# Kernel optimization log

Hardware: AMD Instinct MI355X
Metric: run time of the kernel (lower is better)

## Reference

```python
import jax, jax.numpy as jnp
import numpy as np

B = 2048   # batch
C = 64     # EEG channels (num_eegch)
T = 125    # time samples -> pool5 -> 25 -> (p=5, 5)
H = 8      # num_heads
L = 6      # num_layers
D = 16     # num_projected_features
QK = 8     # qkv_len
P = 5      # tokens before cls
EPS = 1e-5


def setup_inputs() -> dict:
    key = jax.random.key(0)
    ks = iter(jax.random.split(key, 64))

    def nrm(shape, s=0.05):
        return jax.random.normal(next(ks), shape, jnp.float32) * s

    return {
        "x": jax.random.normal(next(ks), (B, 1, C, T), jnp.float32),
        "conv_t_w": nrm((8, 1, 1, 63)),
        "conv_t_b": nrm((8,)),
        "bn1_g": 1.0 + nrm((8,)),
        "bn1_b": nrm((8,)),
        "bn1_m": nrm((8,)),
        "bn1_v": 1.0 + 0.1 * jax.random.uniform(next(ks), (8,), jnp.float32),
        "conv_s_w": nrm((16, 1, C, 1)),
        "conv_s_b": nrm((16,)),
        "bn2_g": 1.0 + nrm((16,)),
        "bn2_b": nrm((16,)),
        "bn2_m": nrm((16,)),
        "bn2_v": 1.0 + 0.1 * jax.random.uniform(next(ks), (16,), jnp.float32),
        "proj_w": nrm((D, 16 * 5)),
        "proj_b": nrm((D,)),
        "cls_token": nrm((1, 1, D), 1.0),
        "pe": nrm((1, P + 1, D), 1.0),
        "qkv_w": nrm((L, 3 * H * QK, D)),
        "qkv_b": nrm((L, 3 * H * QK)),
        "out_w": nrm((L, D, H * QK)),
        "out_b": nrm((L, D)),
        "ln1_g": jnp.ones((L, D), jnp.float32),
        "ln1_b": jnp.zeros((L, D), jnp.float32),
        "ln2_g": jnp.ones((L, D), jnp.float32),
        "ln2_b": jnp.zeros((L, D), jnp.float32),
        "mlp_w1": nrm((L, 2 * D, D)),
        "mlp_b1": nrm((L, 2 * D)),
        "mlp_w2": nrm((L, D, 2 * D)),
        "mlp_b2": nrm((L, D)),
        "head_ln_g": jnp.ones((D,), jnp.float32),
        "head_ln_b": jnp.zeros((D,), jnp.float32),
        "head_w": nrm((2, D)),
        "head_b": nrm((2,)),
    }


def _bn(z, g, b, m, v):
    s = (g * jax.lax.rsqrt(v + EPS))[None, :, None, None]
    return (z - m[None, :, None, None]) * s + b[None, :, None, None]


def _ln(z, g, b):
    m = z.mean(-1, keepdims=True)
    var = jnp.mean((z - m) ** 2, -1, keepdims=True)
    return (z - m) * jax.lax.rsqrt(var + EPS) * g + b


def _forward(x, conv_t_w, conv_t_b, bn1_g, bn1_b, bn1_m, bn1_v,
             conv_s_w, conv_s_b, bn2_g, bn2_b, bn2_m, bn2_v,
             proj_w, proj_b, cls_token, pe,
             qkv_w, qkv_b, out_w, out_b, ln1_g, ln1_b, ln2_g, ln2_b,
             mlp_w1, mlp_b1, mlp_w2, mlp_b2,
             head_ln_g, head_ln_b, head_w, head_b):
    b = x.shape[0]
    dn = ('NCHW', 'OIHW', 'NCHW')
    # temporal conv, 'same' padding on width (kernel 63 -> pad 31/31)
    y = jax.lax.conv_general_dilated(x, conv_t_w, (1, 1), [(0, 0), (31, 31)], dimension_numbers=dn)
    y = _bn(y + conv_t_b[None, :, None, None], bn1_g, bn1_b, bn1_m, bn1_v)
    # grouped spatial conv collapses the EEG-channel axis
    y = jax.lax.conv_general_dilated(y, conv_s_w, (1, 1), 'VALID', dimension_numbers=dn, feature_group_count=8)
    y = _bn(y + conv_s_b[None, :, None, None], bn2_g, bn2_b, bn2_m, bn2_v)
    y = jax.nn.elu(y)                              # (b,16,1,125)
    y = y.reshape(b, 16, 1, T // 5, 5).mean(-1)    # avg_pool2d (1,5) -> (b,16,1,25)
    # dropout: identity at inference
    y = y.reshape(b, 16, 1, P, 5)
    y = jnp.swapaxes(y, 3, 4)
    tok = jnp.swapaxes(y.reshape(b, 16 * 5, P), 1, 2)   # (b,5,80)
    tok = tok @ proj_w.T + proj_b                       # (b,5,16)
    z = jnp.concatenate([jnp.broadcast_to(cls_token, (b, 1, D)), tok], axis=1) + pe  # (b,6,16)
    scale = QK ** -0.5
    for i in range(L):
        h1 = _ln(z, ln1_g[i], ln1_b[i])
        qkv = h1 @ qkv_w[i].T + qkv_b[i]                # (b,6,3*H*QK)
        q, k, v = jnp.split(qkv, 3, axis=-1)
        q = q.reshape(b, P + 1, H, QK).transpose(0, 2, 1, 3)
        k = k.reshape(b, P + 1, H, QK).transpose(0, 2, 1, 3)
        v = v.reshape(b, P + 1, H, QK).transpose(0, 2, 1, 3)
        att = jax.nn.softmax(jnp.einsum('bhsd,bhtd->bhst', q, k) * scale, axis=-1)
        o = jnp.einsum('bhst,bhtd->bhsd', att, v).transpose(0, 2, 1, 3).reshape(b, P + 1, H * QK)
        z = o @ out_w[i].T + out_b[i] + z
        h2 = _ln(z, ln2_g[i], ln2_b[i])
        m = jax.nn.gelu(h2 @ mlp_w1[i].T + mlp_b1[i], approximate=False) @ mlp_w2[i].T + mlp_b2[i]
        z = m + z
    cls = _ln(z[:, 0, :], head_ln_g, head_ln_b)
    return jax.nn.softmax(cls @ head_w.T + head_b, axis=-1)


def reference(x, conv_t_w, conv_t_b, bn1_g, bn1_b, bn1_m, bn1_v,
              conv_s_w, conv_s_b, bn2_g, bn2_b, bn2_m, bn2_v,
              proj_w, proj_b, cls_token, pe,
              qkv_w, qkv_b, out_w, out_b, ln1_g, ln1_b, ln2_g, ln2_b,
              mlp_w1, mlp_b1, mlp_w2, mlp_b2,
              head_ln_g, head_ln_b, head_w, head_b):
    return _forward(x, conv_t_w, conv_t_b, bn1_g, bn1_b, bn1_m, bn1_v,
                    conv_s_w, conv_s_b, bn2_g, bn2_b, bn2_m, bn2_v,
                    proj_w, proj_b, cls_token, pe,
                    qkv_w, qkv_b, out_w, out_b, ln1_g, ln1_b, ln2_g, ln2_b,
                    mlp_w1, mlp_b1, mlp_w2, mlp_b2,
                    head_ln_g, head_ln_b, head_w, head_b)
```

## Files before the change

kernel.cpp:

```cpp
#include <hip/hip_runtime.h>

#define TB 256

#define WAVE_SYNC() do { asm volatile("" ::: "memory"); \
                         __builtin_amdgcn_wave_barrier(); \
                         asm volatile("" ::: "memory"); } while (0)

#define WQKV 0
#define BQKV 3840
#define WOUT 4032
#define BOUT 5120
#define WM1  5136
#define BM1  5776
#define WM2  5808
#define BM2  6384
#define LN1G 6400
#define LN1B 6416
#define LN2G 6432
#define LN2B 6448
#define WEND 6464
#define SSTR 1568
#define SH1  0
#define SQKV 128
#define SMHS 1312
#define LDS_TOT (WEND + 2*SSTR)
#define FSTR 3664
#define FXSP  0
#define FPOOL 3136
#define FTOK  3584

__device__ __forceinline__ float ln_norm16(float z, float g, float bb) {
    float s = z, q = z * z;
    #pragma unroll
    for (int off = 8; off >= 1; off >>= 1) {
        s += __shfl_xor(s, off, 16);
        q += __shfl_xor(q, off, 16);
    }
    float mean = s * 0.0625f;
    float var  = q * 0.0625f - mean * mean;
    return (z - mean) * rsqrtf(var + 1e-5f) * g + bb;
}

__device__ __forceinline__ float gelu_exact(float a) {
    float xa = fabsf(a) * 0.70710678118654752f;
    float tt = 1.f / (1.f + 0.3275911f * xa);
    float poly = tt * (0.254829592f + tt * (-0.284496736f + tt * (1.421413741f
               + tt * (-1.453152027f + tt * 1.061405429f))));
    float erfv = 1.f - poly * __expf(-xa * xa);
    erfv = a >= 0.f ? erfv : -erfv;
    return 0.5f * a * (1.f + erfv);
}

__device__ __forceinline__ float dot16(const float* h, float4 w0, float4 w1,
                                       float4 w2, float4 w3) {
    return h[0]*w0.x + h[1]*w0.y + h[2]*w0.z + h[3]*w0.w
         + h[4]*w1.x + h[5]*w1.y + h[6]*w1.z + h[7]*w1.w
         + h[8]*w2.x + h[9]*w2.y + h[10]*w2.z + h[11]*w2.w
         + h[12]*w3.x + h[13]*w3.y + h[14]*w3.z + h[15]*w3.w;
}

extern "C" __global__ __launch_bounds__(TB, 2)
void eegnet_vit_fused(
    const float* __restrict__ x,
    const float* __restrict__ conv_t_w, const float* __restrict__ conv_t_b,
    const float* __restrict__ bn1_g, const float* __restrict__ bn1_b,
    const float* __restrict__ bn1_m, const float* __restrict__ bn1_v,
    const float* __restrict__ conv_s_w, const float* __restrict__ conv_s_b,
    const float* __restrict__ bn2_g, const float* __restrict__ bn2_b,
    const float* __restrict__ bn2_m, const float* __restrict__ bn2_v,
    const float* __restrict__ proj_w, const float* __restrict__ proj_b,
    const float* __restrict__ cls_token, const float* __restrict__ pe,
    const float* __restrict__ qkv_w, const float* __restrict__ qkv_b,
    const float* __restrict__ out_w, const float* __restrict__ out_b,
    const float* __restrict__ ln1_g, const float* __restrict__ ln1_b,
    const float* __restrict__ ln2_g, const float* __restrict__ ln2_b,
    const float* __restrict__ mlp_w1, const float* __restrict__ mlp_b1,
    const float* __restrict__ mlp_w2, const float* __restrict__ mlp_b2,
    const float* __restrict__ head_ln_g, const float* __restrict__ head_ln_b,
    const float* __restrict__ head_w, const float* __restrict__ head_b,
    float* __restrict__ out)
{
    __shared__ __align__(16) float sm[LDS_TOT];
    const int tid = threadIdx.x;
    const int ss  = tid >> 7;
    const int u   = tid & 127;
    const int b2  = blockIdx.x * 2 + ss;
    float* smf = sm + ss * FSTR;

    for (int i = u; i < 16 * 71; i += 128) {
        int row = i / 71, k = i - row * 71;
        int off = (k < 32) ? k : (k + 125);
        smf[FXSP + row * 196 + off] = 0.f;
    }

    {
        const float* xb = x + (size_t)b2 * 8000;
        const int t = min(u, 124);
        float a0[16];
        #pragma unroll
        for (int o = 0; o < 16; ++o) a0[o] = 0.f;
        #pragma unroll 8
        for (int c = 0; c < 64; ++c) {
            float xv = xb[c * 125 + t];
            #pragma unroll
            for (int o = 0; o < 16; ++o)
                a0[o] += conv_s_w[o * 64 + c] * xv;
        }
        if (u < 125) {
            #pragma unroll
            for (int o = 0; o < 16; ++o)
                smf[FXSP + o * 196 + 32 + t] = a0[o];
        }
    }

    const int oo = u & 15, qg = u >> 4, gg = oo >> 1;
    float sa, cc;
    {
        float s1 = bn1_g[gg] * rsqrtf(bn1_v[gg] + 1e-5f);
        float b1 = (conv_t_b[gg] - bn1_m[gg]) * s1 + bn1_b[gg];
        float s2 = bn2_g[oo] * rsqrtf(bn2_v[oo] + 1e-5f);
        float ssum = 0.f;
        const float4* csw = reinterpret_cast<const float4*>(conv_s_w + oo * 64);
        #pragma unroll
        for (int i = 0; i < 16; ++i) {
            float4 v = csw[i];
            ssum += v.x + v.y + v.z + v.w;
        }
        sa = s1 * s2;
        cc = (b1 * ssum + conv_s_b[oo] - bn2_m[oo]) * s2 + bn2_b[oo];
    }
    float wt[63];
    #pragma unroll
    for (int k = 0; k < 63; ++k) wt[k] = conv_t_w[gg * 63 + k];

    __syncthreads();

    #pragma unroll 1
    for (int jj = 0; jj < 4; ++jj) {
        int j = qg + 8 * jj;
        if (j < 25) {
            int base = FXSP + oo * 196 + 5 * j + 1;
            float acc5[5] = {0.f, 0.f, 0.f, 0.f, 0.f};
            #pragma unroll
            for (int m = 0; m < 67; ++m) {
                float xv = smf[base + m];
                #pragma unroll
                for (int uu = 0; uu < 5; ++uu)
                    if (uu <= m && m - uu <= 62) acc5[uu] += wt[m - uu] * xv;
            }
            float psum = 0.f;
            #pragma unroll
            for (int uu = 0; uu < 5; ++uu) {
                float v = acc5[uu] * sa + cc;
                psum += (v > 0.f) ? v : (__expf(v) - 1.f);
            }
            smf[FPOOL + oo * 28 + j] = psum * 0.2f;
        }
    }

    __syncthreads();

    if (u < 80) {
        int p = u >> 4, dd = u & 15;
        float acc = proj_b[dd];
        const float4* wp = reinterpret_cast<const float4*>(proj_w + dd * 80);
        #pragma unroll
        for (int i = 0; i < 20; ++i) {
            float4 w4 = wp[i];
            acc += w4.x * smf[FPOOL + ((4*i+0)/5) * 28 + p * 5 + ((4*i+0)%5)];
            acc += w4.y * smf[FPOOL + ((4*i+1)/5) * 28 + p * 5 + ((4*i+1)%5)];
            acc += w4.z * smf[FPOOL + ((4*i+2)/5) * 28 + p * 5 + ((4*i+2)%5)];
            acc += w4.w * smf[FPOOL + ((4*i+3)/5) * 28 + p * 5 + ((4*i+3)%5)];
        }
        smf[FTOK + p * 16 + dd] = acc;
    }

    __syncthreads();

    const int d16 = u & 15;
    const int t6c = min(qg, 5);
    float z = ((t6c == 0) ? cls_token[d16] : smf[FTOK + (t6c - 1) * 16 + d16])
            + pe[t6c * 16 + d16];

    const int sb   = WEND + ss * SSTR;
    const int wav  = u >> 6;
    const int al   = u & 63;

    #pragma unroll 1
    for (int li = 0; li < 6; ++li) {
        __syncthreads();

        {
            const float4* s1 = reinterpret_cast<const float4*>(qkv_w + li * 3072);
            #pragma unroll
            for (int it = 0; it < 3; ++it) {
                int i = tid + it * 256;
                float4 v = s1[i];
                int j = i >> 2, k = (i & 3) << 2;
                *reinterpret_cast<float4*>(&sm[WQKV + j * 20 + k]) = v;
            }
            {
                float4 v = reinterpret_cast<const float4*>(out_w + li * 1024)[tid];
                int j = tid >> 4, k = (tid & 15) << 2;
                *reinterpret_cast<float4*>(&sm[WOUT + j * 68 + k]) = v;
            }
            if (tid < 128) {
                float4 v = reinterpret_cast<const float4*>(mlp_w1 + li * 512)[tid];
                int j = tid >> 2, k = (tid & 3) << 2;
                *reinterpret_cast<float4*>(&sm[WM1 + j * 20 + k]) = v;
            } else {
                int i = tid - 128;
                float4 v = reinterpret_cast<const float4*>(mlp_w2 + li * 512)[i];
                int j = i >> 3, k = (i & 7) << 2;
                *reinterpret_cast<float4*>(&sm[WM2 + j * 36 + k]) = v;
            }
            if (tid < 192) sm[BQKV + tid] = qkv_b[li * 192 + tid];
            else if (tid < 208) sm[BOUT + tid - 192] = out_b[li * 16 + tid - 192];
            else if (tid < 240) sm[BM1 + tid - 208]  = mlp_b1[li * 32 + tid - 208];
            else               sm[BM2 + tid - 240]  = mlp_b2[li * 16 + tid - 240];
            if (tid >= 64 && tid < 80)        sm[LN1G + tid - 64]  = ln1_g[li * 16 + tid - 64];
            else if (tid >= 80 && tid < 96)   sm[LN1B + tid - 80]  = ln1_b[li * 16 + tid - 80];
            else if (tid >= 96 && tid < 112)  sm[LN2G + tid - 96]  = ln2_g[li * 16 + tid - 96];
            else if (tid >= 112 && tid < 128) sm[LN2B + tid - 112] = ln2_b[li * 16 + tid - 112];
        }
        __syncthreads();

        sm[sb + SH1 + t6c * 20 + d16] = ln_norm16(z, sm[LN1G + d16], sm[LN1B + d16]);
        WAVE_SYNC();

        float hr[16];
        {
            const float4* pA = reinterpret_cast<const float4*>(&sm[sb + SH1 + t6c * 20]);
            #pragma unroll
            for (int i = 0; i < 4; ++i) {
                float4 va = pA[i];
                hr[4*i+0] = va.x; hr[4*i+1] = va.y; hr[4*i+2] = va.z; hr[4*i+3] = va.w;
            }
        }

        #pragma unroll 2
        for (int r = 0; r < 12; ++r) {
            int j = d16 + 16 * r;
            const float4* wp = reinterpret_cast<const float4*>(&sm[WQKV + j * 20]);
            float4 w0 = wp[0], w1_ = wp[1], w2_ = wp[2], w3_ = wp[3];
            sm[sb + SQKV + t6c * 196 + j] = sm[BQKV + j] + dot16(hr, w0, w1_, w2_, w3_);
        }
        __syncthreads();

        {
            bool act = (wav == 0) ? (al < 32) : (al < 16);
            if (act) {
                int h  = al & 7;
                int qs = (wav == 0) ? (al >> 3) : 4 + (al >> 3);
                const int qoff = sb + SQKV + qs * 196 + h * 8;
                const float4* qp = reinterpret_cast<const float4*>(&sm[qoff]);
                float4 q0 = qp[0], q1 = qp[1];
                float sc[6];
                #pragma unroll
                for (int t = 0; t < 6; ++t) {
                    const float4* kp = reinterpret_cast<const float4*>(&sm[sb + SQKV + t * 196 + 64 + h * 8]);
                    float4 k0 = kp[0], k1 = kp[1];
                    sc[t] = (q0.x*k0.x + q0.y*k0.y + q0.z*k0.z + q0.w*k0.w
                           + q1.x*k1.x + q1.y*k1.y + q1.z*k1.z + q1.w*k1.w)
                           * 0.35355339059327373f;
                }
                float mx = sc[0];
                #pragma unroll
                for (int t = 1; t < 6; ++t) mx = fmaxf(mx, sc[t]);
                float ssum = 0.f;
                #pragma unroll
                for (int t = 0; t < 6; ++t) { sc[t] = __expf(sc[t] - mx); ssum += sc[t]; }
                float inv = 1.f / ssum;
                float o0=0.f,o1=0.f,o2=0.f,o3=0.f,o4=0.f,o5=0.f,o6=0.f,o7=0.f;
                #pragma unroll
                for (int t = 0; t < 6; ++t) {
                    const float4* vp = reinterpret_cast<const float4*>(&sm[sb + SQKV + t * 196 + 128 + h * 8]);
                    float4 v0 = vp[0], v1 = vp[1];
                    float a = sc[t] * inv;
                    o0 += a*v0.x; o1 += a*v0.y; o2 += a*v0.z; o3 += a*v0.w;
                    o4 += a*v1.x; o5 += a*v1.y; o6 += a*v1.z; o7 += a*v1.w;
                }
                *reinterpret_cast<float4*>(&sm[qoff    ]) = float4{o0,o1,o2,o3};
                *reinterpret_cast<float4*>(&sm[qoff + 4]) = float4{o4,o5,o6,o7};
            }
        }
        WAVE_SYNC();

        {
            const float4* wop = reinterpret_cast<const float4*>(&sm[WOUT + d16 * 68]);
            const float4* oa  = reinterpret_cast<const float4*>(&sm[sb + SQKV + t6c * 196]);
            float acc = sm[BOUT + d16];
            #pragma unroll 4
            for (int i = 0; i < 16; ++i) {
                float4 w = wop[i];
                float4 va = oa[i];
                acc += va.x*w.x + va.y*w.y + va.z*w.z + va.w*w.w;
            }
            z += acc;
        }

        sm[sb + SH1 + t6c * 20 + d16] = ln_norm16(z, sm[LN2G + d16], sm[LN2B + d16]);
        WAVE_SYNC();
        {
            const float4* pA = reinterpret_cast<const float4*>(&sm[sb + SH1 + t6c * 20]);
            #pragma unroll
            for (int i = 0; i < 4; ++i) {
                float4 va = pA[i];
                hr[4*i+0] = va.x; hr[4*i+1] = va.y; hr[4*i+2] = va.z; hr[4*i+3] = va.w;
            }
        }

        #pragma unroll
        for (int r = 0; r < 2; ++r) {
            int uu = d16 + 16 * r;
            const float4* wp = reinterpret_cast<const float4*>(&sm[WM1 + uu * 20]);
            float4 w0 = wp[0], w1_ = wp[1], w2_ = wp[2], w3_ = wp[3];
            float a = sm[BM1 + uu] + dot16(hr, w0, w1_, w2_, w3_);
            sm[sb + SMHS + t6c * 36 + uu] = gelu_exact(a);
        }
        WAVE_SYNC();

        {
            const float4* wp = reinterpret_cast<const float4*>(&sm[WM2 + d16 * 36]);
            const float4* mA = reinterpret_cast<const float4*>(&sm[sb + SMHS + t6c * 36]);
            float acc = sm[BM2 + d16];
            #pragma unroll
            for (int i = 0; i < 8; ++i) {
                float4 w = wp[i];
                float4 va = mA[i];
                acc += va.x*w.x + va.y*w.y + va.z*w.z + va.w*w.w;
            }
            z += acc;
        }
    }

    if (u < 16) {
        float cv = ln_norm16(z, head_ln_g[d16], head_ln_b[d16]);
        float p0 = cv * head_w[d16];
        float p1 = cv * head_w[16 + d16];
        #pragma unroll
        for (int off = 8; off >= 1; off >>= 1) {
            p0 += __shfl_xor(p0, off, 16);
            p1 += __shfl_xor(p1, off, 16);
        }
        if (u == 0) {
            float l0 = p0 + head_b[0], l1 = p1 + head_b[1];
            float mx = fmaxf(l0, l1);
            float e0 = __expf(l0 - mx), e1 = __expf(l1 - mx);
            float inv = 1.f / (e0 + e1);
            out[b2 * 2 + 0] = e0 * inv;
            out[b2 * 2 + 1] = e1 * inv;
        }
    }
}

extern "C" void kernel_launch(void* const* d_in, const int* in_sizes, int n_in,
                              void* d_out, int out_size, void* d_ws, size_t ws_size,
                              hipStream_t stream) {
    (void)n_in; (void)d_ws; (void)ws_size; (void)out_size;
    const float* a0  = (const float*)d_in[0];
    const float* a1  = (const float*)d_in[1];
    const float* a2  = (const float*)d_in[2];
    const float* a3  = (const float*)d_in[3];
    const float* a4  = (const float*)d_in[4];
    const float* a5  = (const float*)d_in[5];
    const float* a6  = (const float*)d_in[6];
    const float* a7  = (const float*)d_in[7];
    const float* a8  = (const float*)d_in[8];
    const float* a9  = (const float*)d_in[9];
    const float* a10 = (const float*)d_in[10];
    const float* a11 = (const float*)d_in[11];
    const float* a12 = (const float*)d_in[12];
    const float* a13 = (const float*)d_in[13];
    const float* a14 = (const float*)d_in[14];
    const float* a15 = (const float*)d_in[15];
    const float* a16 = (const float*)d_in[16];
    const float* a17 = (const float*)d_in[17];
    const float* a18 = (const float*)d_in[18];
    const float* a19 = (const float*)d_in[19];
    const float* a20 = (const float*)d_in[20];
    const float* a21 = (const float*)d_in[21];
    const float* a22 = (const float*)d_in[22];
    const float* a23 = (const float*)d_in[23];
    const float* a24 = (const float*)d_in[24];
    const float* a25 = (const float*)d_in[25];
    const float* a26 = (const float*)d_in[26];
    const float* a27 = (const float*)d_in[27];
    const float* a28 = (const float*)d_in[28];
    const float* a29 = (const float*)d_in[29];
    const float* a30 = (const float*)d_in[30];
    const float* a31 = (const float*)d_in[31];
    const float* a32 = (const float*)d_in[32];

    int Bn = in_sizes[0] / (64 * 125);
    eegnet_vit_fused<<<Bn / 2, TB, 0, stream>>>(
        a0, a1, a2, a3, a4, a5, a6, a7, a8, a9, a10, a11, a12, a13, a14, a15, a16,
        a17, a18, a19, a20, a21, a22, a23, a24, a25, a26, a27, a28, a29, a30, a31, a32,
        (float*)d_out);
}
```

Baseline: 248.4 us.

## Split frontend into separate kernel and process two samples per thread in transformer

The fused kernel becomes two launches. A frontend kernel with one sample per 128-thread block writes projected tokens to workspace. A transformer kernel then handles four samples per 256-thread block, with each thread computing two samples so every weight read from LDS is reused twice. The goal is to amortize the per-layer weight staging into LDS and the shared-memory weight reads over more samples, and to size each stage's occupancy on its own. The cost is an extra launch, a global round trip for the tokens, and higher register pressure from keeping two sample states per thread.

```diff
diff --git a/kernel.cpp b/kernel.cpp
--- a/kernel.cpp
+++ b/kernel.cpp
@@ -1,10 +1,147 @@
 #include <hip/hip_runtime.h>
-
-#define TB 256
 
 #define WAVE_SYNC() do { asm volatile("" ::: "memory"); \
                          __builtin_amdgcn_wave_barrier(); \
                          asm volatile("" ::: "memory"); } while (0)
+
+__device__ __forceinline__ float ln_norm16(float z, float g, float bb) {
+    float s = z, q = z * z;
+    #pragma unroll
+    for (int off = 8; off >= 1; off >>= 1) {
+        s += __shfl_xor(s, off, 16);
+        q += __shfl_xor(q, off, 16);
+    }
+    float mean = s * 0.0625f;
+    float var  = q * 0.0625f - mean * mean;
+    return (z - mean) * rsqrtf(var + 1e-5f) * g + bb;
+}
+
+__device__ __forceinline__ float gelu_exact(float a) {
+    float xa = fabsf(a) * 0.70710678118654752f;
+    float tt = 1.f / (1.f + 0.3275911f * xa);
+    float poly = tt * (0.254829592f + tt * (-0.284496736f + tt * (1.421413741f
+               + tt * (-1.453152027f + tt * 1.061405429f))));
+    float erfv = 1.f - poly * __expf(-xa * xa);
+    erfv = a >= 0.f ? erfv : -erfv;
+    return 0.5f * a * (1.f + erfv);
+}
+
+__device__ __forceinline__ float dot16(const float* h, float4 w0, float4 w1,
+                                       float4 w2, float4 w3) {
+    return h[0]*w0.x + h[1]*w0.y + h[2]*w0.z + h[3]*w0.w
+         + h[4]*w1.x + h[5]*w1.y + h[6]*w1.z + h[7]*w1.w
+         + h[8]*w2.x + h[9]*w2.y + h[10]*w2.z + h[11]*w2.w
+         + h[12]*w3.x + h[13]*w3.y + h[14]*w3.z + h[15]*w3.w;
+}
+
+#define FXSP  0
+#define FPOOL 3136
+#define F_TOT 3584
+
+extern "C" __global__ __launch_bounds__(128, 2)
+void eegnet_frontend(
+    const float* __restrict__ x,
+    const float* __restrict__ conv_t_w, const float* __restrict__ conv_t_b,
+    const float* __restrict__ bn1_g, const float* __restrict__ bn1_b,
+    const float* __restrict__ bn1_m, const float* __restrict__ bn1_v,
+    const float* __restrict__ conv_s_w, const float* __restrict__ conv_s_b,
+    const float* __restrict__ bn2_g, const float* __restrict__ bn2_b,
+    const float* __restrict__ bn2_m, const float* __restrict__ bn2_v,
+    const float* __restrict__ proj_w, const float* __restrict__ proj_b,
+    float* __restrict__ tokws)
+{
+    __shared__ __align__(16) float sm[F_TOT];
+    const int b   = blockIdx.x;
+    const int tid = threadIdx.x;
+
+    for (int i = tid; i < 16 * 71; i += 128) {
+        int row = i / 71, k = i - row * 71;
+        int off = (k < 32) ? k : (k + 125);
+        sm[FXSP + row * 196 + off] = 0.f;
+    }
+
+    {
+        const float* xb = x + (size_t)b * 8000;
+        const int t = min(tid, 124);
+        float a0[16];
+        #pragma unroll
+        for (int o = 0; o < 16; ++o) a0[o] = 0.f;
+        #pragma unroll 8
+        for (int c = 0; c < 64; ++c) {
+            float xv = xb[c * 125 + t];
+            #pragma unroll
+            for (int o = 0; o < 16; ++o)
+                a0[o] += conv_s_w[o * 64 + c] * xv;
+        }
+        if (tid < 125) {
+            #pragma unroll
+            for (int o = 0; o < 16; ++o)
+                sm[FXSP + o * 196 + 32 + t] = a0[o];
+        }
+    }
+
+    const int oo = tid & 15, qg = tid >> 4, gg = oo >> 1;
+    float sa, cc;
+    {
+        float s1 = bn1_g[gg] * rsqrtf(bn1_v[gg] + 1e-5f);
+        float b1 = (conv_t_b[gg] - bn1_m[gg]) * s1 + bn1_b[gg];
+        float s2 = bn2_g[oo] * rsqrtf(bn2_v[oo] + 1e-5f);
+        float ssum = 0.f;
+        const float4* csw = reinterpret_cast<const float4*>(conv_s_w + oo * 64);
+        #pragma unroll
+        for (int i = 0; i < 16; ++i) {
+            float4 v = csw[i];
+            ssum += v.x + v.y + v.z + v.w;
+        }
+        sa = s1 * s2;
+        cc = (b1 * ssum + conv_s_b[oo] - bn2_m[oo]) * s2 + bn2_b[oo];
+    }
+    float wt[63];
+    #pragma unroll
+    for (int k = 0; k < 63; ++k) wt[k] = conv_t_w[gg * 63 + k];
+
+    __syncthreads();
+
+    #pragma unroll 1
+    for (int jj = 0; jj < 4; ++jj) {
+        int j = qg + 8 * jj;
+        if (j < 25) {
+            int base = FXSP + oo * 196 + 5 * j + 1;
+            float acc5[5] = {0.f, 0.f, 0.f, 0.f, 0.f};
+            #pragma unroll
+            for (int m = 0; m < 67; ++m) {
+                float xv = sm[base + m];
+                #pragma unroll
+                for (int uu = 0; uu < 5; ++uu)
+                    if (uu <= m && m - uu <= 62) acc5[uu] += wt[m - uu] * xv;
+            }
+            float psum = 0.f;
+            #pragma unroll
+            for (int uu = 0; uu < 5; ++uu) {
+                float v = acc5[uu] * sa + cc;
+                psum += (v > 0.f) ? v : (__expf(v) - 1.f);
+            }
+            sm[FPOOL + oo * 28 + j] = psum * 0.2f;
+        }
+    }
+
+    __syncthreads();
+
+    if (tid < 80) {
+        int p = tid >> 4, dd = tid & 15;
+        float acc = proj_b[dd];
+        const float4* wp = reinterpret_cast<const float4*>(proj_w + dd * 80);
+        #pragma unroll
+        for (int i = 0; i < 20; ++i) {
+            float4 w4 = wp[i];
+            acc += w4.x * sm[FPOOL + ((4*i+0)/5) * 28 + p * 5 + ((4*i+0)%5)];
+            acc += w4.y * sm[FPOOL + ((4*i+1)/5) * 28 + p * 5 + ((4*i+1)%5)];
+            acc += w4.z * sm[FPOOL + ((4*i+2)/5) * 28 + p * 5 + ((4*i+2)%5)];
+            acc += w4.w * sm[FPOOL + ((4*i+3)/5) * 28 + p * 5 + ((4*i+3)%5)];
+        }
+        tokws[b * 80 + tid] = acc;
+    }
+}
 
 #define WQKV 0
 #define BQKV 3840
@@ -23,52 +160,10 @@
 #define SH1  0
 #define SQKV 128
 #define SMHS 1312
-#define LDS_TOT (WEND + 2*SSTR)
-#define FSTR 3664
-#define FXSP  0
-#define FPOOL 3136
-#define FTOK  3584
-
-__device__ __forceinline__ float ln_norm16(float z, float g, float bb) {
-    float s = z, q = z * z;
-    #pragma unroll
-    for (int off = 8; off >= 1; off >>= 1) {
-        s += __shfl_xor(s, off, 16);
-        q += __shfl_xor(q, off, 16);
-    }
-    float mean = s * 0.0625f;
-    float var  = q * 0.0625f - mean * mean;
-    return (z - mean) * rsqrtf(var + 1e-5f) * g + bb;
-}
-
-__device__ __forceinline__ float gelu_exact(float a) {
-    float xa = fabsf(a) * 0.70710678118654752f;
-    float tt = 1.f / (1.f + 0.3275911f * xa);
-    float poly = tt * (0.254829592f + tt * (-0.284496736f + tt * (1.421413741f
-               + tt * (-1.453152027f + tt * 1.061405429f))));
-    float erfv = 1.f - poly * __expf(-xa * xa);
-    erfv = a >= 0.f ? erfv : -erfv;
-    return 0.5f * a * (1.f + erfv);
-}
-
-__device__ __forceinline__ float dot16(const float* h, float4 w0, float4 w1,
-                                       float4 w2, float4 w3) {
-    return h[0]*w0.x + h[1]*w0.y + h[2]*w0.z + h[3]*w0.w
-         + h[4]*w1.x + h[5]*w1.y + h[6]*w1.z + h[7]*w1.w
-         + h[8]*w2.x + h[9]*w2.y + h[10]*w2.z + h[11]*w2.w
-         + h[12]*w3.x + h[13]*w3.y + h[14]*w3.z + h[15]*w3.w;
-}
-
-extern "C" __global__ __launch_bounds__(TB, 2)
-void eegnet_vit_fused(
-    const float* __restrict__ x,
-    const float* __restrict__ conv_t_w, const float* __restrict__ conv_t_b,
-    const float* __restrict__ bn1_g, const float* __restrict__ bn1_b,
-    const float* __restrict__ bn1_m, const float* __restrict__ bn1_v,
-    const float* __restrict__ conv_s_w, const float* __restrict__ conv_s_b,
-    const float* __restrict__ bn2_g, const float* __restrict__ bn2_b,
-    const float* __restrict__ bn2_m, const float* __restrict__ bn2_v,
-    const float* __restrict__ proj_w, const float* __restrict__ proj_b,
+#define T_TOT (WEND + 4*SSTR)
+
+extern "C" __global__ __launch_bounds__(256, 2)
+void eegnet_transformer(
     const float* __restrict__ cls_token, const float* __restrict__ pe,
     const float* __restrict__ qkv_w, const float* __restrict__ qkv_b,
     const float* __restrict__ out_w, const float* __restrict__ out_b,
@@ -78,113 +173,30 @@
     const float* __restrict__ mlp_w2, const float* __restrict__ mlp_b2,
     const float* __restrict__ head_ln_g, const float* __restrict__ head_ln_b,
     const float* __restrict__ head_w, const float* __restrict__ head_b,
-    float* __restrict__ out)
+    const float* __restrict__ tokws, float* __restrict__ out)
 {
-    __shared__ __align__(16) float sm[LDS_TOT];
+    __shared__ __align__(16) float sm[T_TOT];
     const int tid = threadIdx.x;
     const int ss  = tid >> 7;
     const int u   = tid & 127;
-    const int b2  = blockIdx.x * 2 + ss;
-    float* smf = sm + ss * FSTR;
-
-    for (int i = u; i < 16 * 71; i += 128) {
-        int row = i / 71, k = i - row * 71;
-        int off = (k < 32) ? k : (k + 125);
-        smf[FXSP + row * 196 + off] = 0.f;
-    }
-
+    const int sA  = blockIdx.x * 4 + ss * 2;
+    const int d16 = u & 15, qg = u >> 4;
+    const int t6c = min(qg, 5);
+    const int wav = u >> 6, al = u & 63;
+    const int sbA = WEND + (ss * 2    ) * SSTR;
+    const int sbB = WEND + (ss * 2 + 1) * SSTR;
+
+    float zA, zB;
     {
-        const float* xb = x + (size_t)b2 * 8000;
-        const int t = min(u, 124);
-        float a0[16];
-        #pragma unroll
-        for (int o = 0; o < 16; ++o) a0[o] = 0.f;
-        #pragma unroll 8
-        for (int c = 0; c < 64; ++c) {
-            float xv = xb[c * 125 + t];
-            #pragma unroll
-            for (int o = 0; o < 16; ++o)
-                a0[o] += conv_s_w[o * 64 + c] * xv;
-        }
-        if (u < 125) {
-            #pragma unroll
-            for (int o = 0; o < 16; ++o)
-                smf[FXSP + o * 196 + 32 + t] = a0[o];
-        }
-    }
-
-    const int oo = u & 15, qg = u >> 4, gg = oo >> 1;
-    float sa, cc;
-    {
-        float s1 = bn1_g[gg] * rsqrtf(bn1_v[gg] + 1e-5f);
-        float b1 = (conv_t_b[gg] - bn1_m[gg]) * s1 + bn1_b[gg];
-        float s2 = bn2_g[oo] * rsqrtf(bn2_v[oo] + 1e-5f);
-        float ssum = 0.f;
-        const float4* csw = reinterpret_cast<const float4*>(conv_s_w + oo * 64);
-        #pragma unroll
-        for (int i = 0; i < 16; ++i) {
-            float4 v = csw[i];
-            ssum += v.x + v.y + v.z + v.w;
-        }
-        sa = s1 * s2;
-        cc = (b1 * ssum + conv_s_b[oo] - bn2_m[oo]) * s2 + bn2_b[oo];
-    }
-    float wt[63];
-    #pragma unroll
-    for (int k = 0; k < 63; ++k) wt[k] = conv_t_w[gg * 63 + k];
-
-    __syncthreads();
-
-    #pragma unroll 1
-    for (int jj = 0; jj < 4; ++jj) {
-        int j = qg + 8 * jj;
-        if (j < 25) {
-            int base = FXSP + oo * 196 + 5 * j + 1;
-            float acc5[5] = {0.f, 0.f, 0.f, 0.f, 0.f};
-            #pragma unroll
-            for (int m = 0; m < 67; ++m) {
-                float xv = smf[base + m];
-                #pragma unroll
-                for (int uu = 0; uu < 5; ++uu)
-                    if (uu <= m && m - uu <= 62) acc5[uu] += wt[m - uu] * xv;
-            }
-            float psum = 0.f;
-            #pragma unroll
-            for (int uu = 0; uu < 5; ++uu) {
-                float v = acc5[uu] * sa + cc;
-                psum += (v > 0.f) ? v : (__expf(v) - 1.f);
-            }
-            smf[FPOOL + oo * 28 + j] = psum * 0.2f;
-        }
-    }
-
-    __syncthreads();
-
-    if (u < 80) {
-        int p = u >> 4, dd = u & 15;
-        float acc = proj_b[dd];
-        const float4* wp = reinterpret_cast<const float4*>(proj_w + dd * 80);
-        #pragma unroll
-        for (int i = 0; i < 20; ++i) {
-            float4 w4 = wp[i];
-            acc += w4.x * smf[FPOOL + ((4*i+0)/5) * 28 + p * 5 + ((4*i+0)%5)];
-            acc += w4.y * smf[FPOOL + ((4*i+1)/5) * 28 + p * 5 + ((4*i+1)%5)];
-            acc += w4.z * smf[FPOOL + ((4*i+2)/5) * 28 + p * 5 + ((4*i+2)%5)];
-            acc += w4.w * smf[FPOOL + ((4*i+3)/5) * 28 + p * 5 + ((4*i+3)%5)];
-        }
-        smf[FTOK + p * 16 + dd] = acc;
-    }
-
-    __syncthreads();
-
-    const int d16 = u & 15;
-    const int t6c = min(qg, 5);
-    float z = ((t6c == 0) ? cls_token[d16] : smf[FTOK + (t6c - 1) * 16 + d16])
-            + pe[t6c * 16 + d16];
-
-    const int sb   = WEND + ss * SSTR;
-    const int wav  = u >> 6;
-    const int al   = u & 63;
+        float peV = pe[t6c * 16 + d16];
+        if (t6c == 0) {
+            float cv = cls_token[d16];
+            zA = cv + peV; zB = cv + peV;
+        } else {
+            zA = tokws[(sA    ) * 80 + (t6c - 1) * 16 + d16] + peV;
+            zB = tokws[(sA + 1) * 80 + (t6c - 1) * 16 + d16] + peV;
+        }
+    }
 
     #pragma unroll 1
     for (int li = 0; li < 6; ++li) {
@@ -225,16 +237,22 @@
         }
         __syncthreads();
 
-        sm[sb + SH1 + t6c * 20 + d16] = ln_norm16(z, sm[LN1G + d16], sm[LN1B + d16]);
+        {
+            float g = sm[LN1G + d16], bb = sm[LN1B + d16];
+            sm[sbA + SH1 + t6c * 20 + d16] = ln_norm16(zA, g, bb);
+            sm[sbB + SH1 + t6c * 20 + d16] = ln_norm16(zB, g, bb);
+        }
         WAVE_SYNC();
 
-        float hr[16];
-        {
-            const float4* pA = reinterpret_cast<const float4*>(&sm[sb + SH1 + t6c * 20]);
+        float hrA[16], hrB[16];
+        {
+            const float4* pA = reinterpret_cast<const float4*>(&sm[sbA + SH1 + t6c * 20]);
+            const float4* pB = reinterpret_cast<const float4*>(&sm[sbB + SH1 + t6c * 20]);
             #pragma unroll
             for (int i = 0; i < 4; ++i) {
-                float4 va = pA[i];
-                hr[4*i+0] = va.x; hr[4*i+1] = va.y; hr[4*i+2] = va.z; hr[4*i+3] = va.w;
+                float4 va = pA[i], vb = pB[i];
+                hrA[4*i+0]=va.x; hrA[4*i+1]=va.y; hrA[4*i+2]=va.z; hrA[4*i+3]=va.w;
+                hrB[4*i+0]=vb.x; hrB[4*i+1]=vb.y; hrB[4*i+2]=vb.z; hrB[4*i+3]=vb.w;
             }
         }
 
@@ -243,7 +261,9 @@
             int j = d16 + 16 * r;
             const float4* wp = reinterpret_cast<const float4*>(&sm[WQKV + j * 20]);
             float4 w0 = wp[0], w1_ = wp[1], w2_ = wp[2], w3_ = wp[3];
-            sm[sb + SQKV + t6c * 196 + j] = sm[BQKV + j] + dot16(hr, w0, w1_, w2_, w3_);
+            float bb = sm[BQKV + j];
+            sm[sbA + SQKV + t6c * 196 + j] = bb + dot16(hrA, w0, w1_, w2_, w3_);
+            sm[sbB + SQKV + t6c * 196 + j] = bb + dot16(hrB, w0, w1_, w2_, w3_);
         }
         __syncthreads();
 
@@ -252,61 +272,84 @@
             if (act) {
                 int h  = al & 7;
                 int qs = (wav == 0) ? (al >> 3) : 4 + (al >> 3);
-                const int qoff = sb + SQKV + qs * 196 + h * 8;
-                const float4* qp = reinterpret_cast<const float4*>(&sm[qoff]);
-                float4 q0 = qp[0], q1 = qp[1];
-                float sc[6];
+                const int qoffA = sbA + SQKV + qs * 196 + h * 8;
+                const int qoffB = sbB + SQKV + qs * 196 + h * 8;
+                const float4* qpA = reinterpret_cast<const float4*>(&sm[qoffA]);
+                const float4* qpB = reinterpret_cast<const float4*>(&sm[qoffB]);
+                float4 qA0 = qpA[0], qA1 = qpA[1], qB0 = qpB[0], qB1 = qpB[1];
+                float scA[6], scB[6];
                 #pragma unroll
                 for (int t = 0; t < 6; ++t) {
-                    const float4* kp = reinterpret_cast<const float4*>(&sm[sb + SQKV + t * 196 + 64 + h * 8]);
-                    float4 k0 = kp[0], k1 = kp[1];
-                    sc[t] = (q0.x*k0.x + q0.y*k0.y + q0.z*k0.z + q0.w*k0.w
-                           + q1.x*k1.x + q1.y*k1.y + q1.z*k1.z + q1.w*k1.w)
-                           * 0.35355339059327373f;
+                    const float4* kA = reinterpret_cast<const float4*>(&sm[sbA + SQKV + t * 196 + 64 + h * 8]);
+                    const float4* kB = reinterpret_cast<const float4*>(&sm[sbB + SQKV + t * 196 + 64 + h * 8]);
+                    float4 a0 = kA[0], a1 = kA[1], b0 = kB[0], b1 = kB[1];
+                    scA[t] = (qA0.x*a0.x + qA0.y*a0.y + qA0.z*a0.z + qA0.w*a0.w
+                            + qA1.x*a1.x + qA1.y*a1.y + qA1.z*a1.z + qA1.w*a1.w)
+                            * 0.35355339059327373f;
+                    scB[t] = (qB0.x*b0.x + qB0.y*b0.y + qB0.z*b0.z + qB0.w*b0.w
+                            + qB1.x*b1.x + qB1.y*b1.y + qB1.z*b1.z + qB1.w*b1.w)
+                            * 0.35355339059327373f;
                 }
-                float mx = sc[0];
+                float mxA = scA[0], mxB = scB[0];
                 #pragma unroll
-                for (int t = 1; t < 6; ++t) mx = fmaxf(mx, sc[t]);
-                float ssum = 0.f;
-                #pragma unroll
-                for (int t = 0; t < 6; ++t) { sc[t] = __expf(sc[t] - mx); ssum += sc[t]; }
-                float inv = 1.f / ssum;
-                float o0=0.f,o1=0.f,o2=0.f,o3=0.f,o4=0.f,o5=0.f,o6=0.f,o7=0.f;
+                for (int t = 1; t < 6; ++t) { mxA = fmaxf(mxA, scA[t]); mxB = fmaxf(mxB, scB[t]); }
+                float suA = 0.f, suB = 0.f;
                 #pragma unroll
                 for (int t = 0; t < 6; ++t) {
-                    const float4* vp = reinterpret_cast<const float4*>(&sm[sb + SQKV + t * 196 + 128 + h * 8]);
-                    float4 v0 = vp[0], v1 = vp[1];
-                    float a = sc[t] * inv;
-                    o0 += a*v0.x; o1 += a*v0.y; o2 += a*v0.z; o3 += a*v0.w;
-                    o4 += a*v1.x; o5 += a*v1.y; o6 += a*v1.z; o7 += a*v1.w;
+                    scA[t] = __expf(scA[t] - mxA); suA += scA[t];
+                    scB[t] = __expf(scB[t] - mxB); suB += scB[t];
                 }
-                *reinterpret_cast<float4*>(&sm[qoff    ]) = float4{o0,o1,o2,o3};
-                *reinterpret_cast<float4*>(&sm[qoff + 4]) = float4{o4,o5,o6,o7};
+                float ivA = 1.f / suA, ivB = 1.f / suB;
+                float oA[8] = {0,0,0,0,0,0,0,0}, oB[8] = {0,0,0,0,0,0,0,0};
+                #pragma unroll
+                for (int t = 0; t < 6; ++t) {
+                    const float4* vA = reinterpret_cast<const float4*>(&sm[sbA + SQKV + t * 196 + 128 + h * 8]);
+                    const float4* vB = reinterpret_cast<const float4*>(&sm[sbB + SQKV + t * 196 + 128 + h * 8]);
+                    float4 a0 = vA[0], a1 = vA[1], b0 = vB[0], b1 = vB[1];
+                    float aa = scA[t] * ivA, ab = scB[t] * ivB;
+                    oA[0]+=aa*a0.x; oA[1]+=aa*a0.y; oA[2]+=aa*a0.z; oA[3]+=aa*a0.w;
+                    oA[4]+=aa*a1.x; oA[5]+=aa*a1.y; oA[6]+=aa*a1.z; oA[7]+=aa*a1.w;
+                    oB[0]+=ab*b0.x; oB[1]+=ab*b0.y; oB[2]+=ab*b0.z; oB[3]+=ab*b0.w;
+                    oB[4]+=ab*b1.x; oB[5]+=ab*b1.y; oB[6]+=ab*b1.z; oB[7]+=ab*b1.w;
+                }
+                *reinterpret_cast<float4*>(&sm[qoffA    ]) = float4{oA[0],oA[1],oA[2],oA[3]};
+                *reinterpret_cast<float4*>(&sm[qoffA + 4]) = float4{oA[4],oA[5],oA[6],oA[7]};
+                *reinterpret_cast<float4*>(&sm[qoffB    ]) = float4{oB[0],oB[1],oB[2],oB[3]};
+                *reinterpret_cast<float4*>(&sm[qoffB + 4]) = float4{oB[4],oB[5],oB[6],oB[7]};
             }
         }
         WAVE_SYNC();
 
         {
             const float4* wop = reinterpret_cast<const float4*>(&sm[WOUT + d16 * 68]);
-            const float4* oa  = reinterpret_cast<const float4*>(&sm[sb + SQKV + t6c * 196]);
-            float acc = sm[BOUT + d16];
+            const float4* oaA = reinterpret_cast<const float4*>(&sm[sbA + SQKV + t6c * 196]);
+            const float4* oaB = reinterpret_cast<const float4*>(&sm[sbB + SQKV + t6c * 196]);
+            float bb = sm[BOUT + d16];
+            float aA = bb, aB = bb;
             #pragma unroll 4
             for (int i = 0; i < 16; ++i) {
                 float4 w = wop[i];
-                float4 va = oa[i];
-                acc += va.x*w.x + va.y*w.y + va.z*w.z + va.w*w.w;
-            }
-            z += acc;
-        }
-
-        sm[sb + SH1 + t6c * 20 + d16] = ln_norm16(z, sm[LN2G + d16], sm[LN2B + d16]);
+                float4 va = oaA[i], vb = oaB[i];
+                aA += va.x*w.x + va.y*w.y + va.z*w.z + va.w*w.w;
+                aB += vb.x*w.x + vb.y*w.y + vb.z*w.z + vb.w*w.w;
+            }
+            zA += aA; zB += aB;
+        }
+
+        {
+            float g = sm[LN2G + d16], bb = sm[LN2B + d16];
+            sm[sbA + SH1 + t6c * 20 + d16] = ln_norm16(zA, g, bb);
+            sm[sbB + SH1 + t6c * 20 + d16] = ln_norm16(zB, g, bb);
+        }
         WAVE_SYNC();
         {
-            const float4* pA = reinterpret_cast<const float4*>(&sm[sb + SH1 + t6c * 20]);
+            const float4* pA = reinterpret_cast<const float4*>(&sm[sbA + SH1 + t6c * 20]);
+            const float4* pB = reinterpret_cast<const float4*>(&sm[sbB + SH1 + t6c * 20]);
             #pragma unroll
             for (int i = 0; i < 4; ++i) {
-                float4 va = pA[i];
-                hr[4*i+0] = va.x; hr[4*i+1] = va.y; hr[4*i+2] = va.z; hr[4*i+3] = va.w;
+                float4 va = pA[i], vb = pB[i];
+                hrA[4*i+0]=va.x; hrA[4*i+1]=va.y; hrA[4*i+2]=va.z; hrA[4*i+3]=va.w;
+                hrB[4*i+0]=vb.x; hrB[4*i+1]=vb.y; hrB[4*i+2]=vb.z; hrB[4*i+3]=vb.w;
             }
         }
 
@@ -315,41 +358,63 @@
             int uu = d16 + 16 * r;
             const float4* wp = reinterpret_cast<const float4*>(&sm[WM1 + uu * 20]);
             float4 w0 = wp[0], w1_ = wp[1], w2_ = wp[2], w3_ = wp[3];
-            float a = sm[BM1 + uu] + dot16(hr, w0, w1_, w2_, w3_);
-            sm[sb + SMHS + t6c * 36 + uu] = gelu_exact(a);
+            float bb = sm[BM1 + uu];
+            float aA = bb + dot16(hrA, w0, w1_, w2_, w3_);
+            float aB = bb + dot16(hrB, w0, w1_, w2_, w3_);
+            sm[sbA + SMHS + t6c * 36 + uu] = gelu_exact(aA);
+            sm[sbB + SMHS + t6c * 36 + uu] = gelu_exact(aB);
         }
         WAVE_SYNC();
 
         {
             const float4* wp = reinterpret_cast<const float4*>(&sm[WM2 + d16 * 36]);
-            const float4* mA = reinterpret_cast<const float4*>(&sm[sb + SMHS + t6c * 36]);
-            float acc = sm[BM2 + d16];
+            const float4* mA = reinterpret_cast<const float4*>(&sm[sbA + SMHS + t6c * 36]);
+            const float4* mB = reinterpret_cast<const float4*>(&sm[sbB + SMHS + t6c * 36]);
+            float bb = sm[BM2 + d16];
+            float aA = bb, aB = bb;
             #pragma unroll
             for (int i = 0; i < 8; ++i) {
                 float4 w = wp[i];
-                float4 va = mA[i];
-                acc += va.x*w.x + va.y*w.y + va.z*w.z + va.w*w.w;
-            }
-            z += acc;
+                float4 va = mA[i], vb = mB[i];
+                aA += va.x*w.x + va.y*w.y + va.z*w.z + va.w*w.w;
+                aB += vb.x*w.x + vb.y*w.y + vb.z*w.z + vb.w*w.w;
+            }
+            zA += aA; zB += aB;
         }
     }
 
     if (u < 16) {
-        float cv = ln_norm16(z, head_ln_g[d16], head_ln_b[d16]);
-        float p0 = cv * head_w[d16];
-        float p1 = cv * head_w[16 + d16];
+        float g = head_ln_g[d16], bb = head_ln_b[d16];
+        float w0 = head_w[d16], w1 = head_w[16 + d16];
+        float cvA = ln_norm16(zA, g, bb);
+        float cvB = ln_norm16(zB, g, bb);
+        float pA0 = cvA * w0, pA1 = cvA * w1;
+        float pB0 = cvB * w0, pB1 = cvB * w1;
         #pragma unroll
         for (int off = 8; off >= 1; off >>= 1) {
-            p0 += __shfl_xor(p0, off, 16);
-            p1 += __shfl_xor(p1, off, 16);
+            pA0 += __shfl_xor(pA0, off, 16);
+            pA1 += __shfl_xor(pA1, off, 16);
+            pB0 += __shfl_xor(pB0, off, 16);
+            pB1 += __shfl_xor(pB1, off, 16);
         }
         if (u == 0) {
-            float l0 = p0 + head_b[0], l1 = p1 + head_b[1];
-            float mx = fmaxf(l0, l1);
-            float e0 = __expf(l0 - mx), e1 = __expf(l1 - mx);
-            float inv = 1.f / (e0 + e1);
-            out[b2 * 2 + 0] = e0 * inv;
-            out[b2 * 2 + 1] = e1 * inv;
+            float hb0 = head_b[0], hb1 = head_b[1];
+            {
+                float l0 = pA0 + hb0, l1 = pA1 + hb1;
+                float mx = fmaxf(l0, l1);
+                float e0 = __expf(l0 - mx), e1 = __expf(l1 - mx);
+                float inv = 1.f / (e0 + e1);
+                out[sA * 2 + 0] = e0 * inv;
+                out[sA * 2 + 1] = e1 * inv;
+            }
+            {
+                float l0 = pB0 + hb0, l1 = pB1 + hb1;
+                float mx = fmaxf(l0, l1);
+                float e0 = __expf(l0 - mx), e1 = __expf(l1 - mx);
+                float inv = 1.f / (e0 + e1);
+                out[(sA + 1) * 2 + 0] = e0 * inv;
+                out[(sA + 1) * 2 + 1] = e1 * inv;
+            }
         }
     }
 }
@@ -357,7 +422,7 @@
 extern "C" void kernel_launch(void* const* d_in, const int* in_sizes, int n_in,
                               void* d_out, int out_size, void* d_ws, size_t ws_size,
                               hipStream_t stream) {
-    (void)n_in; (void)d_ws; (void)ws_size; (void)out_size;
+    (void)n_in; (void)ws_size; (void)out_size;
     const float* a0  = (const float*)d_in[0];
     const float* a1  = (const float*)d_in[1];
     const float* a2  = (const float*)d_in[2];
@@ -393,8 +458,12 @@
     const float* a32 = (const float*)d_in[32];
 
     int Bn = in_sizes[0] / (64 * 125);
-    eegnet_vit_fused<<<Bn / 2, TB, 0, stream>>>(
-        a0, a1, a2, a3, a4, a5, a6, a7, a8, a9, a10, a11, a12, a13, a14, a15, a16,
-        a17, a18, a19, a20, a21, a22, a23, a24, a25, a26, a27, a28, a29, a30, a31, a32,
-        (float*)d_out);
-}
+    float* tokws = (float*)d_ws;
+
+    eegnet_frontend<<<Bn, 128, 0, stream>>>(
+        a0, a1, a2, a3, a4, a5, a6, a7, a8, a9, a10, a11, a12, a13, a14, tokws);
+
+    eegnet_transformer<<<Bn / 4, 256, 0, stream>>>(
+        a15, a16, a17, a18, a19, a20, a21, a22, a23, a24, a25, a26, a27, a28,
+        a29, a30, a31, a32, tokws, (float*)d_out);
+}
```

Measured after the change: 242.9 us. 1.02x faster.
